# Optimization experiments

Hardware: AMD Instinct MI355X
Metric: run time of the kernel (lower is better)

## Reference

```python
import jax, jax.numpy as jnp
import numpy as np

H = 256
SLOTS = 64
EPS = 1e-5


def setup_inputs() -> dict:
    key = jax.random.key(0)
    ks = jax.random.split(key, 10)
    B, T = 4096, 128
    # original feeds integer-valued floats in [0,10)
    x = jax.random.randint(ks[0], (B, T, 1), 0, 10).astype(jnp.float32)
    s = 0.02
    return {
        "x": x,
        "W_embed": jax.random.normal(ks[1], (1, H), jnp.float32) * s,
        "b_embed": jnp.zeros((H,), jnp.float32),
        "W_update": jax.random.normal(ks[2], (H, H), jnp.float32) * s,
        "b_update": jnp.zeros((H,), jnp.float32),
        "gamma": jnp.ones((H,), jnp.float32),
        "beta": jnp.zeros((H,), jnp.float32),
        "W_out": jax.random.normal(ks[3], (H, 10), jnp.float32) * s,
        "b_out": jnp.zeros((10,), jnp.float32),
        "context_strength": jnp.asarray(0.2, jnp.float32),
    }


def _layernorm(h, gamma, beta):
    mu = jnp.mean(h, axis=-1, keepdims=True)
    var = jnp.mean(jnp.square(h - mu), axis=-1, keepdims=True)
    return (h - mu) * jax.lax.rsqrt(var + EPS) * gamma + beta


def reference(x, W_embed, b_embed, W_update, b_update, gamma, beta, W_out, b_out, context_strength):
    B, T, _ = x.shape
    cs = jax.nn.sigmoid(context_strength)
    h0 = jnp.zeros((B, H), x.dtype)
    mem0 = jnp.zeros((B, SLOTS, H), x.dtype)
    ptrs = jnp.arange(T, dtype=jnp.int32) % SLOTS  # pointer is identical across batch
    xs = (jnp.transpose(x, (1, 0, 2)), ptrs)        # [T,B,1], [T]

    def step(carry, inputs):
        h, mem = carry
        xt, ptr = inputs
        inp = jnp.tanh(xt @ W_embed + b_embed)          # [B,H]
        context = jax.lax.dynamic_slice_in_dim(mem, ptr, 1, axis=1)[:, 0, :]  # gather slot
        combined = inp + cs * context
        h = jnp.tanh((combined + h) @ W_update + b_update)
        h = _layernorm(h, gamma, beta)
        mem = jax.lax.dynamic_update_slice_in_dim(mem, h[:, None, :], ptr, axis=1)
        return (h, mem), None

    (h, _), _ = jax.lax.scan(step, (h0, mem0), xs)
    return h @ W_out + b_out
```

## Files before the change

### kernel.cpp

```cpp
#include <hip/hip_runtime.h>
#include <hip/hip_bf16.h>
#include <hip/hip_fp16.h>
#include <stdint.h>

#define H 256
#define BT 4096
#define TS 128
#define ROWS 16
#define NBLK 256
#define NTH 1024
#define LD 260
#define LDP 264

typedef __attribute__((ext_vector_type(8))) _Float16 f16x8;
typedef __attribute__((ext_vector_type(4))) float f32x4;

__device__ __forceinline__ float exp2_fast(float x){ float r; asm("v_exp_f32 %0, %1" : "=v"(r) : "v"(x)); return r; }
__device__ __forceinline__ float rcp_fast(float x){ float r; asm("v_rcp_f32 %0, %1" : "=v"(r) : "v"(x)); return r; }
__device__ __forceinline__ float rsq_fast(float x){ float r; asm("v_rsq_f32 %0, %1" : "=v"(r) : "v"(x)); return r; }
__device__ __forceinline__ float tanh_fast(float x){
  float e = exp2_fast(x * 2.8853900817779268f);
  return 1.0f - 2.0f * rcp_fast(e + 1.0f);
}
__device__ __forceinline__ unsigned pk_f16(float a, float b){
  __half2 h2 = __float22half2_rn(make_float2(a, b));
  union { __half2 h; unsigned u; } cv; cv.h = h2; return cv.u;
}
__device__ __forceinline__ float f16_lo_f32(unsigned v){
  float r; asm("v_cvt_f32_f16 %0, %1" : "=v"(r) : "v"(v)); return r;
}
__device__ __forceinline__ unsigned pk_bf16(float a, float b){
  __hip_bfloat162 h2 = __float22bfloat162_rn(make_float2(a, b));
  union { __hip_bfloat162 h; unsigned u; } cv; cv.h = h2; return cv.u;
}
__device__ __forceinline__ void bar_lgkm(){ asm volatile("s_waitcnt lgkmcnt(0)\n\ts_barrier" ::: "memory"); }

template<int CTRL>
__device__ __forceinline__ float dpp_add(float x){
  int y = __builtin_amdgcn_update_dpp(0, __float_as_int(x), CTRL, 0xf, 0xf, false);
  return x + __int_as_float(y);
}
#define ROR1 0x121
#define ROR2 0x122
#define ROR4 0x124
#define ROR8 0x128
#define BC15 0x142
#define BC31 0x143
__device__ __forceinline__ float lane_f(float v, int n){
  return __int_as_float(__builtin_amdgcn_readlane(__float_as_int(v), n));
}

__global__ __launch_bounds__(NTH, 4) void wp_kernel(
    const float* __restrict__ x, const float* __restrict__ We, const float* __restrict__ be,
    const float* __restrict__ Wu, const float* __restrict__ bu, const float* __restrict__ gm,
    const float* __restrict__ bt, const float* __restrict__ Wo, const float* __restrict__ bo,
    const float* __restrict__ cst, unsigned short* __restrict__ hist, float* __restrict__ out,
    int use_hist)
{
  __shared__ __align__(16) float emb[10][LD];
  __shared__ __align__(16) unsigned hp[8][LDP];
  __shared__ __align__(16) float hfin[ROWS][LDP];
  __shared__ __align__(16) unsigned short afrag[8][64][8];
  __shared__ unsigned char xidx[ROWS][TS];

  const int tid = threadIdx.x;
  const int r0 = blockIdx.x * ROWS;
  const int w  = tid >> 6;
  const int l  = tid & 63;
  const int fr = l & 15;
  const int fo = l >> 4;
  const int c0 = 16*w + fr;
  const int rp = w >> 1;
  const int sh = (w & 1) << 4;

  float cs;
  { float c = cst[0]; cs = rcp_fast(1.0f + exp2_fast(-c * 1.4426950408889634f)); }

  for (int i = tid; i < ROWS*TS; i += NTH) {
    int r = i >> 7, t = i & 127;
    xidx[r][t] = (unsigned char)(int)(x[((size_t)(r0 + r))*TS + t] + 0.5f);
  }
  for (int i = tid; i < 10*H; i += NTH) {
    int v = i >> 8, k = i & 255;
    emb[v][k] = tanh_fast((float)v * We[k] + be[k]);
  }

  f16x8 wf[8];
  #pragma unroll
  for (int kc = 0; kc < 8; ++kc) {
    #pragma unroll
    for (int i = 0; i < 8; ++i) {
      int kg = 32*kc + 8*fo + i;
      wf[kc][i] = (_Float16)Wu[(size_t)kg*H + c0];
    }
  }
  const float bval = bu[c0];
  f32x4 g4 = *(const f32x4*)(gm + 4*l);
  f32x4 b4 = *(const f32x4*)(bt + 4*l);

  const int XR = l ^ (2*fo);
  const int wkc = l >> 3, wfo = (l >> 1) & 3, we = l & 1;
  unsigned short* const aw = &afrag[wkc][(w + 16*wfo) ^ wkc ^ (2*wfo)][4*we];
  const unsigned* const hpr = &hp[rp][4*l];
  const unsigned char* const xr = &xidx[w][0];
  const size_t histLane = (size_t)(r0 + w)*H + 4*l;
  __syncthreads();

  {
    int xv = xr[0];
    f32x4 e4 = *(const f32x4*)&emb[xv][4*l];
    uint2 p = { pk_f16(e4[0], e4[1]), pk_f16(e4[2], e4[3]) };
    *(uint2*)aw = p;
  }
  __syncthreads();

  uint2 cP = {0,0}, cQ = {0,0};

#define PHASE2() do { \
    f32x4 acc = {bval, bval, bval, bval}; \
    _Pragma("unroll") \
    for (int kc = 0; kc < 8; ++kc) { \
      f16x8 af = *(const f16x8*)&afrag[kc][XR ^ kc][0]; \
      acc = __builtin_amdgcn_mfma_f32_16x16x32_f16(af, wf[kc], acc, 0, 0, 0); \
    } \
    hp[2*fo  ][c0] = pk_f16(tanh_fast(acc[0]), tanh_fast(acc[1])); \
    hp[2*fo+1][c0] = pk_f16(tanh_fast(acc[2]), tanh_fast(acc[3])); \
  } while(0)

#define LN_STATS_HV() \
    uint4 qv = *(const uint4*)hpr; \
    float h0 = f16_lo_f32(qv.x >> sh); \
    float h1 = f16_lo_f32(qv.y >> sh); \
    float h2 = f16_lo_f32(qv.z >> sh); \
    float h3 = f16_lo_f32(qv.w >> sh); \
    float s1 = (h0+h1) + (h2+h3); \
    float s2 = h0*h0; \
    s2 = fmaf(h1,h1,s2); s2 = fmaf(h2,h2,s2); s2 = fmaf(h3,h3,s2); \
    s1 = dpp_add<ROR1>(s1); s1 = dpp_add<ROR2>(s1); s1 = dpp_add<ROR4>(s1); s1 = dpp_add<ROR8>(s1); \
    s2 = dpp_add<ROR1>(s2); s2 = dpp_add<ROR2>(s2); s2 = dpp_add<ROR4>(s2); s2 = dpp_add<ROR8>(s2); \
    s1 = dpp_add<BC15>(s1); s1 = dpp_add<BC31>(s1); \
    s2 = dpp_add<BC15>(s2); s2 = dpp_add<BC31>(s2); \
    float S1 = lane_f(s1, 63); \
    float S2 = lane_f(s2, 63); \
    float mu  = S1 * 0.00390625f; \
    float var = S2 * 0.00390625f - mu*mu; \
    float rs  = rsq_fast(var + 1e-5f); \
    float hv0 = fmaf(h0-mu, rs*g4[0], b4[0]); \
    float hv1 = fmaf(h1-mu, rs*g4[1], b4[1]); \
    float hv2 = fmaf(h2-mu, rs*g4[2], b4[2]); \
    float hv3 = fmaf(h3-mu, rs*g4[3], b4[3]);

#define PHASE3(HW, CUSE, CLOAD, tt) do { \
    int xv = xr[(tt)+1]; \
    f32x4 e4 = *(const f32x4*)&emb[xv][4*l]; \
    LN_STATS_HV(); \
    float a0, a1, a2, a3; \
    if ((CUSE) && use_hist) { \
      a0 = fmaf(cs, __uint_as_float(cP.x << 16),         e4[0] + hv0); \
      a1 = fmaf(cs, __uint_as_float(cP.x & 0xffff0000u), e4[1] + hv1); \
      a2 = fmaf(cs, __uint_as_float(cP.y << 16),         e4[2] + hv2); \
      a3 = fmaf(cs, __uint_as_float(cP.y & 0xffff0000u), e4[3] + hv3); \
    } else { \
      a0 = e4[0] + hv0; a1 = e4[1] + hv1; a2 = e4[2] + hv2; a3 = e4[3] + hv3; \
    } \
    uint2 pkk = { pk_f16(a0,a1), pk_f16(a2,a3) }; \
    *(uint2*)aw = pkk; \
    if ((HW) && use_hist) { \
      uint2 hb = { pk_bf16(hv0,hv1), pk_bf16(hv2,hv3) }; \
      *(uint2*)(hist + (size_t)(tt)*(BT*H) + histLane) = hb; \
    } \
    if ((CUSE) || (CLOAD)) { cP = cQ; } \
    if ((CLOAD) && use_hist) \
      cQ = *(const uint2*)(hist + (size_t)((tt)-61)*(BT*H) + histLane); \
  } while(0)

  for (int t = 0; t < 61; ++t)  { PHASE2(); bar_lgkm(); PHASE3(1,0,0,t); bar_lgkm(); }
  for (int t = 61; t < 63; ++t) { PHASE2(); bar_lgkm(); PHASE3(1,0,1,t); bar_lgkm(); }
  {                               PHASE2(); bar_lgkm(); PHASE3(1,1,1,63); bar_lgkm(); }
  for (int t = 64; t < 125; ++t){ PHASE2(); bar_lgkm(); PHASE3(0,1,1,t); bar_lgkm(); }
  for (int t = 125; t < 127; ++t){PHASE2(); bar_lgkm(); PHASE3(0,1,0,t); bar_lgkm(); }
  {
    PHASE2(); bar_lgkm();
    LN_STATS_HV();
    f32x4 o = {hv0, hv1, hv2, hv3};
    *(f32x4*)&hfin[w][4*l] = o;
  }

  __syncthreads();
  if (tid < ROWS * 10) {
    int r = tid / 10, c = tid % 10;
    float acc = bo[c];
    for (int k = 0; k < H; ++k) acc += hfin[r][k] * Wo[k*10 + c];
    out[((size_t)(r0 + r))*10 + c] = acc;
  }
}

extern "C" void kernel_launch(void* const* d_in, const int* in_sizes, int n_in,
                              void* d_out, int out_size, void* d_ws, size_t ws_size,
                              hipStream_t stream) {
  const float* x   = (const float*)d_in[0];
  const float* We  = (const float*)d_in[1];
  const float* be  = (const float*)d_in[2];
  const float* Wu  = (const float*)d_in[3];
  const float* bu  = (const float*)d_in[4];
  const float* gm  = (const float*)d_in[5];
  const float* bt  = (const float*)d_in[6];
  const float* Wo  = (const float*)d_in[7];
  const float* bo  = (const float*)d_in[8];
  const float* cst = (const float*)d_in[9];
  float* out = (float*)d_out;

  size_t need = (size_t)64 * BT * H * sizeof(unsigned short);
  int use_hist = (ws_size >= need) ? 1 : 0;

  hipLaunchKernelGGL(wp_kernel, dim3(NBLK), dim3(NTH), 0, stream,
                     x, We, be, Wu, bu, gm, bt, Wo, bo, cst,
                     (unsigned short*)d_ws, out, use_hist);
}
```

Before: 145.2 us.

## Specialize warps into separate MFMA and LayerNorm groups per timestep

Splits the 16 waves into two roles. Waves 0-7 each compute two 16-column MFMA tiles of the recurrent matmul. Waves 8-15 each handle LayerNorm, context mixing and history I/O for two rows. Previously every wave did both phases for one column tile and one row. The aim is lower per-wave register pressure and less instruction work per phase. The cost is that half the waves sit idle during each phase, so the serialized per-step critical path may grow.

```diff
diff --git a/kernel.cpp b/kernel.cpp
--- a/kernel.cpp
+++ b/kernel.cpp
@@ -26,7 +26,7 @@
   __half2 h2 = __float22half2_rn(make_float2(a, b));
   union { __half2 h; unsigned u; } cv; cv.h = h2; return cv.u;
 }
-__device__ __forceinline__ float f16_lo_f32(unsigned v){
+__device__ __forceinline__ float f16_lo(unsigned v){
   float r; asm("v_cvt_f32_f16 %0, %1" : "=v"(r) : "v"(v)); return r;
 }
 __device__ __forceinline__ unsigned pk_bf16(float a, float b){
@@ -49,6 +49,9 @@
 __device__ __forceinline__ float lane_f(float v, int n){
   return __int_as_float(__builtin_amdgcn_readlane(__float_as_int(v), n));
 }
+#define CHAIN(s) do { \
+    s = dpp_add<ROR1>(s); s = dpp_add<ROR2>(s); s = dpp_add<ROR4>(s); s = dpp_add<ROR8>(s); \
+    s = dpp_add<BC15>(s); s = dpp_add<BC31>(s); } while(0)
 
 __global__ __launch_bounds__(NTH, 4) void wp_kernel(
     const float* __restrict__ x, const float* __restrict__ We, const float* __restrict__ be,
@@ -69,9 +72,8 @@
   const int l  = tid & 63;
   const int fr = l & 15;
   const int fo = l >> 4;
-  const int c0 = 16*w + fr;
-  const int rp = w >> 1;
-  const int sh = (w & 1) << 4;
+  const bool isG = (w < 8);
+  const int  li  = w & 7;
 
   float cs;
   { float c = cst[0]; cs = rcp_fast(1.0f + exp2_fast(-c * 1.4426950408889634f)); }
@@ -85,105 +87,150 @@
     emb[v][k] = tanh_fast((float)v * We[k] + be[k]);
   }
 
-  f16x8 wf[8];
-  #pragma unroll
-  for (int kc = 0; kc < 8; ++kc) {
+  const int c0 = 32*li + fr, c1 = c0 + 16;
+  f16x8 wf0[8], wf1[8];
+  float bval0 = 0.f, bval1 = 0.f;
+  if (isG) {
     #pragma unroll
-    for (int i = 0; i < 8; ++i) {
-      int kg = 32*kc + 8*fo + i;
-      wf[kc][i] = (_Float16)Wu[(size_t)kg*H + c0];
+    for (int kc = 0; kc < 8; ++kc) {
+      #pragma unroll
+      for (int i = 0; i < 8; ++i) {
+        int kg = 32*kc + 8*fo + i;
+        wf0[kc][i] = (_Float16)Wu[(size_t)kg*H + c0];
+        wf1[kc][i] = (_Float16)Wu[(size_t)kg*H + c1];
+      }
     }
-  }
-  const float bval = bu[c0];
-  f32x4 g4 = *(const f32x4*)(gm + 4*l);
-  f32x4 b4 = *(const f32x4*)(bt + 4*l);
-
+    bval0 = bu[c0]; bval1 = bu[c1];
+  }
+
+  const int re = 2*li, ro = re + 1;
+  f32x4 g4 = {0,0,0,0}, b4 = {0,0,0,0};
+  if (!isG) {
+    g4 = *(const f32x4*)(gm + 4*l);
+    b4 = *(const f32x4*)(bt + 4*l);
+  }
+  const int wkc = l >> 3, wfo = (l >> 1) & 3, we = l & 1;
+  unsigned short* const awE = &afrag[wkc][(re + 16*wfo) ^ wkc ^ (2*wfo)][4*we];
+  unsigned short* const awO = &afrag[wkc][(ro + 16*wfo) ^ wkc ^ (2*wfo)][4*we];
+  const unsigned* const hpr = &hp[li][4*l];
+  const unsigned char* const xrE = &xidx[re][0];
+  const unsigned char* const xrO = &xidx[ro][0];
+  const size_t histLaneE = (size_t)(r0 + re)*H + 4*l;
+  const size_t histLaneO = (size_t)(r0 + ro)*H + 4*l;
   const int XR = l ^ (2*fo);
-  const int wkc = l >> 3, wfo = (l >> 1) & 3, we = l & 1;
-  unsigned short* const aw = &afrag[wkc][(w + 16*wfo) ^ wkc ^ (2*wfo)][4*we];
-  const unsigned* const hpr = &hp[rp][4*l];
-  const unsigned char* const xr = &xidx[w][0];
-  const size_t histLane = (size_t)(r0 + w)*H + 4*l;
   __syncthreads();
 
-  {
-    int xv = xr[0];
+  if (!isG) {
+    int xv = xrE[0];
     f32x4 e4 = *(const f32x4*)&emb[xv][4*l];
     uint2 p = { pk_f16(e4[0], e4[1]), pk_f16(e4[2], e4[3]) };
-    *(uint2*)aw = p;
+    *(uint2*)awE = p;
+    xv = xrO[0];
+    e4 = *(const f32x4*)&emb[xv][4*l];
+    uint2 q = { pk_f16(e4[0], e4[1]), pk_f16(e4[2], e4[3]) };
+    *(uint2*)awO = q;
   }
   __syncthreads();
 
-  uint2 cP = {0,0}, cQ = {0,0};
+  uint2 cPe = {0,0}, cQe = {0,0}, cPo = {0,0}, cQo = {0,0};
 
 #define PHASE2() do { \
-    f32x4 acc = {bval, bval, bval, bval}; \
+    f32x4 acc0 = {bval0, bval0, bval0, bval0}; \
+    f32x4 acc1 = {bval1, bval1, bval1, bval1}; \
     _Pragma("unroll") \
     for (int kc = 0; kc < 8; ++kc) { \
       f16x8 af = *(const f16x8*)&afrag[kc][XR ^ kc][0]; \
-      acc = __builtin_amdgcn_mfma_f32_16x16x32_f16(af, wf[kc], acc, 0, 0, 0); \
-    } \
-    hp[2*fo  ][c0] = pk_f16(tanh_fast(acc[0]), tanh_fast(acc[1])); \
-    hp[2*fo+1][c0] = pk_f16(tanh_fast(acc[2]), tanh_fast(acc[3])); \
+      acc0 = __builtin_amdgcn_mfma_f32_16x16x32_f16(af, wf0[kc], acc0, 0, 0, 0); \
+      acc1 = __builtin_amdgcn_mfma_f32_16x16x32_f16(af, wf1[kc], acc1, 0, 0, 0); \
+    } \
+    hp[2*fo  ][c0] = pk_f16(tanh_fast(acc0[0]), tanh_fast(acc0[1])); \
+    hp[2*fo+1][c0] = pk_f16(tanh_fast(acc0[2]), tanh_fast(acc0[3])); \
+    hp[2*fo  ][c1] = pk_f16(tanh_fast(acc1[0]), tanh_fast(acc1[1])); \
+    hp[2*fo+1][c1] = pk_f16(tanh_fast(acc1[2]), tanh_fast(acc1[3])); \
   } while(0)
 
-#define LN_STATS_HV() \
+#define LN2() \
     uint4 qv = *(const uint4*)hpr; \
-    float h0 = f16_lo_f32(qv.x >> sh); \
-    float h1 = f16_lo_f32(qv.y >> sh); \
-    float h2 = f16_lo_f32(qv.z >> sh); \
-    float h3 = f16_lo_f32(qv.w >> sh); \
-    float s1 = (h0+h1) + (h2+h3); \
-    float s2 = h0*h0; \
-    s2 = fmaf(h1,h1,s2); s2 = fmaf(h2,h2,s2); s2 = fmaf(h3,h3,s2); \
-    s1 = dpp_add<ROR1>(s1); s1 = dpp_add<ROR2>(s1); s1 = dpp_add<ROR4>(s1); s1 = dpp_add<ROR8>(s1); \
-    s2 = dpp_add<ROR1>(s2); s2 = dpp_add<ROR2>(s2); s2 = dpp_add<ROR4>(s2); s2 = dpp_add<ROR8>(s2); \
-    s1 = dpp_add<BC15>(s1); s1 = dpp_add<BC31>(s1); \
-    s2 = dpp_add<BC15>(s2); s2 = dpp_add<BC31>(s2); \
-    float S1 = lane_f(s1, 63); \
-    float S2 = lane_f(s2, 63); \
-    float mu  = S1 * 0.00390625f; \
-    float var = S2 * 0.00390625f - mu*mu; \
-    float rs  = rsq_fast(var + 1e-5f); \
-    float hv0 = fmaf(h0-mu, rs*g4[0], b4[0]); \
-    float hv1 = fmaf(h1-mu, rs*g4[1], b4[1]); \
-    float hv2 = fmaf(h2-mu, rs*g4[2], b4[2]); \
-    float hv3 = fmaf(h3-mu, rs*g4[3], b4[3]);
+    float he0 = f16_lo(qv.x),       he1 = f16_lo(qv.y),       he2 = f16_lo(qv.z),       he3 = f16_lo(qv.w); \
+    float ho0 = f16_lo(qv.x >> 16), ho1 = f16_lo(qv.y >> 16), ho2 = f16_lo(qv.z >> 16), ho3 = f16_lo(qv.w >> 16); \
+    float s1e = (he0+he1) + (he2+he3); \
+    float s2e = he0*he0; s2e = fmaf(he1,he1,s2e); s2e = fmaf(he2,he2,s2e); s2e = fmaf(he3,he3,s2e); \
+    float s1o = (ho0+ho1) + (ho2+ho3); \
+    float s2o = ho0*ho0; s2o = fmaf(ho1,ho1,s2o); s2o = fmaf(ho2,ho2,s2o); s2o = fmaf(ho3,ho3,s2o); \
+    CHAIN(s1e); CHAIN(s2e); CHAIN(s1o); CHAIN(s2o); \
+    float mue  = lane_f(s1e,63) * 0.00390625f; \
+    float vare = lane_f(s2e,63) * 0.00390625f - mue*mue; \
+    float rse  = rsq_fast(vare + 1e-5f); \
+    float muo  = lane_f(s1o,63) * 0.00390625f; \
+    float varo = lane_f(s2o,63) * 0.00390625f - muo*muo; \
+    float rso  = rsq_fast(varo + 1e-5f); \
+    float hve0 = fmaf(he0-mue, rse*g4[0], b4[0]); \
+    float hve1 = fmaf(he1-mue, rse*g4[1], b4[1]); \
+    float hve2 = fmaf(he2-mue, rse*g4[2], b4[2]); \
+    float hve3 = fmaf(he3-mue, rse*g4[3], b4[3]); \
+    float hvo0 = fmaf(ho0-muo, rso*g4[0], b4[0]); \
+    float hvo1 = fmaf(ho1-muo, rso*g4[1], b4[1]); \
+    float hvo2 = fmaf(ho2-muo, rso*g4[2], b4[2]); \
+    float hvo3 = fmaf(ho3-muo, rso*g4[3], b4[3]);
 
 #define PHASE3(HW, CUSE, CLOAD, tt) do { \
-    int xv = xr[(tt)+1]; \
-    f32x4 e4 = *(const f32x4*)&emb[xv][4*l]; \
-    LN_STATS_HV(); \
-    float a0, a1, a2, a3; \
+    int xve = xrE[(tt)+1], xvo = xrO[(tt)+1]; \
+    f32x4 ee = *(const f32x4*)&emb[xve][4*l]; \
+    f32x4 eo = *(const f32x4*)&emb[xvo][4*l]; \
+    LN2(); \
+    float a0, a1, a2, a3, d0, d1, d2, d3; \
     if ((CUSE) && use_hist) { \
-      a0 = fmaf(cs, __uint_as_float(cP.x << 16),         e4[0] + hv0); \
-      a1 = fmaf(cs, __uint_as_float(cP.x & 0xffff0000u), e4[1] + hv1); \
-      a2 = fmaf(cs, __uint_as_float(cP.y << 16),         e4[2] + hv2); \
-      a3 = fmaf(cs, __uint_as_float(cP.y & 0xffff0000u), e4[3] + hv3); \
+      a0 = fmaf(cs, __uint_as_float(cPe.x << 16),         ee[0] + hve0); \
+      a1 = fmaf(cs, __uint_as_float(cPe.x & 0xffff0000u), ee[1] + hve1); \
+      a2 = fmaf(cs, __uint_as_float(cPe.y << 16),         ee[2] + hve2); \
+      a3 = fmaf(cs, __uint_as_float(cPe.y & 0xffff0000u), ee[3] + hve3); \
+      d0 = fmaf(cs, __uint_as_float(cPo.x << 16),         eo[0] + hvo0); \
+      d1 = fmaf(cs, __uint_as_float(cPo.x & 0xffff0000u), eo[1] + hvo1); \
+      d2 = fmaf(cs, __uint_as_float(cPo.y << 16),         eo[2] + hvo2); \
+      d3 = fmaf(cs, __uint_as_float(cPo.y & 0xffff0000u), eo[3] + hvo3); \
     } else { \
-      a0 = e4[0] + hv0; a1 = e4[1] + hv1; a2 = e4[2] + hv2; a3 = e4[3] + hv3; \
-    } \
-    uint2 pkk = { pk_f16(a0,a1), pk_f16(a2,a3) }; \
-    *(uint2*)aw = pkk; \
+      a0 = ee[0] + hve0; a1 = ee[1] + hve1; a2 = ee[2] + hve2; a3 = ee[3] + hve3; \
+      d0 = eo[0] + hvo0; d1 = eo[1] + hvo1; d2 = eo[2] + hvo2; d3 = eo[3] + hvo3; \
+    } \
+    uint2 pe = { pk_f16(a0,a1), pk_f16(a2,a3) }; \
+    *(uint2*)awE = pe; \
+    uint2 po = { pk_f16(d0,d1), pk_f16(d2,d3) }; \
+    *(uint2*)awO = po; \
     if ((HW) && use_hist) { \
-      uint2 hb = { pk_bf16(hv0,hv1), pk_bf16(hv2,hv3) }; \
-      *(uint2*)(hist + (size_t)(tt)*(BT*H) + histLane) = hb; \
-    } \
-    if ((CUSE) || (CLOAD)) { cP = cQ; } \
-    if ((CLOAD) && use_hist) \
-      cQ = *(const uint2*)(hist + (size_t)((tt)-61)*(BT*H) + histLane); \
+      uint2 hbe = { pk_bf16(hve0,hve1), pk_bf16(hve2,hve3) }; \
+      *(uint2*)(hist + (size_t)(tt)*(BT*H) + histLaneE) = hbe; \
+      uint2 hbo = { pk_bf16(hvo0,hvo1), pk_bf16(hvo2,hvo3) }; \
+      *(uint2*)(hist + (size_t)(tt)*(BT*H) + histLaneO) = hbo; \
+    } \
+    if ((CUSE) || (CLOAD)) { cPe = cQe; cPo = cQo; } \
+    if ((CLOAD) && use_hist) { \
+      cQe = *(const uint2*)(hist + (size_t)((tt)-61)*(BT*H) + histLaneE); \
+      cQo = *(const uint2*)(hist + (size_t)((tt)-61)*(BT*H) + histLaneO); \
+    } \
   } while(0)
 
-  for (int t = 0; t < 61; ++t)  { PHASE2(); bar_lgkm(); PHASE3(1,0,0,t); bar_lgkm(); }
-  for (int t = 61; t < 63; ++t) { PHASE2(); bar_lgkm(); PHASE3(1,0,1,t); bar_lgkm(); }
-  {                               PHASE2(); bar_lgkm(); PHASE3(1,1,1,63); bar_lgkm(); }
-  for (int t = 64; t < 125; ++t){ PHASE2(); bar_lgkm(); PHASE3(0,1,1,t); bar_lgkm(); }
-  for (int t = 125; t < 127; ++t){PHASE2(); bar_lgkm(); PHASE3(0,1,0,t); bar_lgkm(); }
+#define STEP(HW, CUSE, CLOAD, tt) do { \
+    if (isG) PHASE2(); \
+    bar_lgkm(); \
+    if (!isG) PHASE3(HW, CUSE, CLOAD, tt); \
+    bar_lgkm(); \
+  } while(0)
+
+  for (int t = 0; t < 61; ++t)   STEP(1,0,0,t);
+  for (int t = 61; t < 63; ++t)  STEP(1,0,1,t);
+                                 STEP(1,1,1,63);
+  for (int t = 64; t < 125; ++t) STEP(0,1,1,t);
+  for (int t = 125; t < 127; ++t)STEP(0,1,0,t);
   {
-    PHASE2(); bar_lgkm();
-    LN_STATS_HV();
-    f32x4 o = {hv0, hv1, hv2, hv3};
-    *(f32x4*)&hfin[w][4*l] = o;
+    if (isG) PHASE2();
+    bar_lgkm();
+    if (!isG) {
+      LN2();
+      f32x4 oe = {hve0, hve1, hve2, hve3};
+      *(f32x4*)&hfin[re][4*l] = oe;
+      f32x4 oo = {hvo0, hvo1, hvo2, hvo3};
+      *(f32x4*)&hfin[ro][4*l] = oo;
+    }
   }
 
   __syncthreads();
```

Result: slower. 227.3 us (+56.5%).
